# Performance work log

Hardware: AMD Instinct MI355X
Metric: run time of the kernel (lower is better)

The kernel has to match this reference:

```python
import jax, jax.numpy as jnp
import numpy as np

C = 256

def conv1x1(x, w, b):
    # pointwise Conv3d(kernel=1): out-channel d from in-channel c
    return jnp.einsum('blhwc,dc->blhwd', x, w) + b

def setup_inputs() -> dict:
    key = jax.random.key(0)
    ks = jax.random.split(key, 20)
    inp = {
        'x': jax.random.normal(ks[0], (2, 8, 64, 64, C + 3), jnp.float32),
        'mask': jnp.ones((2, 8, 64, 64), dtype=bool),
        'spatial_correction_matrix': jax.random.normal(ks[1], (2, 8, 4, 4), jnp.float32),
    }
    scale = 1.0 / np.sqrt(C)
    names = ['sq', 'sk', 'sv', 'tq', 'tk', 'tv']
    for i, n in enumerate(names):
        inp[n + '_w'] = jax.random.normal(ks[2 + 2 * i], (C, C), jnp.float32) * scale
        inp[n + '_b'] = jax.random.normal(ks[3 + 2 * i], (C,), jnp.float32) * 0.01
    inp['s_gamma'] = jax.random.normal(ks[14], (1,), jnp.float32) * 0.1
    inp['t_gamma'] = jax.random.normal(ks[15], (1,), jnp.float32) * 0.1
    return inp

def reference(x, mask, spatial_correction_matrix,
              sq_w, sq_b, sk_w, sk_b, sv_w, sv_b, s_gamma,
              tq_w, tq_b, tk_w, tk_b, tv_w, tv_b, t_gamma):
    x_s = x[..., :-3]                      # (B,L,H,W,C)
    B, L, H, W, Ch = x_s.shape
    prev = x_s                             # last_time == None -> last_time = x.detach()
    HW = H * W

    # ---- SpatialAttention: channel-attention (CxC) per (B,L) slice ----
    q = jnp.transpose(conv1x1(x_s, sq_w, sq_b), (0, 1, 4, 2, 3)).reshape(B * L, Ch, HW)
    k = jnp.transpose(conv1x1(x_s, sk_w, sk_b), (0, 1, 4, 2, 3)).reshape(B * L, Ch, HW)
    attn = jax.nn.softmax(jnp.einsum('bcs,bds->bcd', q, k), axis=-1)   # (BL,C,C)
    v = jnp.transpose(conv1x1(x_s, sv_w, sv_b), (0, 1, 4, 2, 3)).reshape(B * L, Ch, HW)
    out = jnp.einsum('bds,bcd->bsc', v, attn).reshape(B, L, H, W, Ch)
    x1 = s_gamma * out + x_s

    # ---- TemporalAttention: query from x1, key/value from prev ----
    q2 = jnp.transpose(conv1x1(x1, tq_w, tq_b), (0, 1, 4, 2, 3)).reshape(B * L, Ch, HW)
    # key: permute(0,2,1,4,3) swaps H/W before flatten (faithful to source)
    k2 = jnp.transpose(conv1x1(prev, tk_w, tk_b), (0, 1, 4, 3, 2)).reshape(B * L, Ch, HW)
    attn2 = jax.nn.softmax(jnp.einsum('bcs,bds->bcd', q2, k2), axis=-1)
    # value: reshape of (B,C,L,H,W)-contiguous tensor into (B*L,C,HW) scrambles C/L (faithful)
    v2 = jnp.transpose(conv1x1(prev, tv_w, tv_b), (0, 4, 1, 2, 3)).reshape(B * L, Ch, HW)
    out2 = jnp.einsum('bds,bcd->bsc', v2, attn2).reshape(B, L, H, W, Ch)
    x2 = t_gamma * out2 + x1
    return x2
```

## Files before the change

kernel.cpp:

```cpp
#include <hip/hip_runtime.h>
#include <stdint.h>


#define S4 4096
#define CH 256

typedef __attribute__((ext_vector_type(8))) short bf16x8;
typedef __attribute__((ext_vector_type(4))) float f32x4;

static __device__ __forceinline__ float bf2f(unsigned short u){
  union { unsigned int i; float f; } v; v.i = ((unsigned int)u) << 16; return v.f;
}
static __device__ __forceinline__ unsigned short f2bf(float f){
  union { float f; unsigned int i; } v; v.f = f;
  unsigned int x = v.i;
  x += 0x7fffu + ((x >> 16) & 1u);
  return (unsigned short)(x >> 16);
}
static __device__ __forceinline__ void gload16(const void* g, void* l){
  __builtin_amdgcn_global_load_lds((const __attribute__((address_space(1))) void*)g,
                                   (__attribute__((address_space(3))) void*)l, 16, 0, 0);
}


// ... 25 lines not shown

__global__ void k_wprep(const float* __restrict__ w0, const float* __restrict__ w1,
                        const float* __restrict__ w2, const float* __restrict__ w3,
                        const float* __restrict__ w4, const float* __restrict__ w5,
                        unsigned short* __restrict__ whi, unsigned short* __restrict__ wlo,
                        unsigned short* __restrict__ wvthi, unsigned short* __restrict__ wvtlo){
  int i = blockIdx.x*256 + threadIdx.x;
  int mat = i >> 16; int off = i & 65535;
  if (mat < 6){
    const float* src = mat==0?w0:mat==1?w1:mat==2?w2:mat==3?w3:mat==4?w4:w5;
    float v = src[off];
    unsigned short h = f2bf(v);
    whi[i] = h;
    wlo[i] = f2bf(v - bf2f(h));
  } else {
    int e = off >> 8, d = off & 255;
    float v = w2[d*256 + e];
    unsigned short h = f2bf(v);
    wvthi[off] = h;
    wvtlo[off] = f2bf(v - bf2f(h));
  }
}

__global__ void k_gcomb(const float* __restrict__ Gp,
                        unsigned short* __restrict__ ghi, unsigned short* __restrict__ glo){
  int bl = blockIdx.y;
  int idx = blockIdx.x*256 + threadIdx.x;
  float s = 0.f;
  #pragma unroll
  for (int p = 0; p < 8; ++p) s += Gp[(long)(bl*8 + p)*65536 + idx];
  unsigned short h = f2bf(s);
  ghi[(long)bl*65536 + idx] = h;
  glo[(long)bl*65536 + idx] = f2bf(s - bf2f(h));
}


template<bool BSWAP>
__global__ __launch_bounds__(256) void k_gram(
  const unsigned short* __restrict__ Xhi, const unsigned short* __restrict__ Xlo,
  float* __restrict__ Gp)
{
  __shared__ char lds[65536];
  char* ldsAh = lds;
  char* ldsAl = lds + 16384;
  char* ldsBh = lds + 32768;
  char* ldsBl = lds + 49152;
// ... 97 lines not shown
      }
    }
    __syncthreads();
    #pragma unroll
    for (int g2 = 0; g2 < 2; ++g2){
      int t2 = g2*256 + tid;
      int rr = t2 >> 4;
      int co = (t2 & 15) * 8;
      int mg = m0 + chv*32 + rr;
      int ng = n0 + co;
      long oidx = (long)zz*65536 + (long)mg*256 + ng;
      float4 o0, o1;
      o0.x = ldsF[rr*136+co+0]; o0.y = ldsF[rr*136+co+1];
      o0.z = ldsF[rr*136+co+2]; o0.w = ldsF[rr*136+co+3];
      o1.x = ldsF[rr*136+co+4]; o1.y = ldsF[rr*136+co+5];
      o1.z = ldsF[rr*136+co+6]; o1.w = ldsF[rr*136+co+7];
      *(float4*)(Gp + oidx)     = o0;
      *(float4*)(Gp + oidx + 4) = o1;
    }
  }
}


__device__ __forceinline__ void mega_tile(
  char* lds, int tid,
  const unsigned short* __restrict__ Ah, const unsigned short* __restrict__ Al,
  const unsigned short* __restrict__ Bh, const unsigned short* __restrict__ Bl,
  f32x4 acc[4][4])
{
  char* ldsAh = lds;
  char* ldsAl = lds + 32768;
  char* ldsBh = lds + 65536;
  char* ldsBl = lds + 81920;
  const int l = tid & 63, wid = tid >> 6;
  const int g = wid >> 2, w2 = wid & 3;
  const int wm = w2 >> 1, wn = w2 & 1;
  const int lm = l & 15, lk = l >> 4;
  const int fm = g*128 + wm*64, fn = wn*64;

  for (int kt = 0; kt < 4; ++kt){
    const int kq = kt << 6;
    #pragma unroll
    for (int it = 0; it < 4; ++it){
      int idx = it*512 + tid;
      int r = idx >> 3;
      int kb = ((idx & 7) << 4) ^ ((r & 7) << 4);
      long ga = (long)r*256 + kq + (kb >> 1);
      gload16(Ah + ga, ldsAh + idx*16);
      gload16(Al + ga, ldsAl + idx*16);
    }
    #pragma unroll
    for (int it = 0; it < 2; ++it){
      int idx = it*512 + tid;
      int r = idx >> 3;
      int kb = ((idx & 7) << 4) ^ ((r & 7) << 4);
      long gb = (long)r*256 + kq + (kb >> 1);
      gload16(Bh + gb, ldsBh + idx*16);
      gload16(Bl + gb, ldsBl + idx*16);
    }
    __syncthreads();
    #pragma unroll
    for (int kk = 0; kk < 2; ++kk){
      bf16x8 ah[4], al_[4];
      #pragma unroll
      for (int i=0;i<4;++i){
        int r = fm + i*16 + lm;
        int kb = ((kk<<6) + (lk<<4)) ^ ((r & 7) << 4);
        ah[i]  = *(const bf16x8*)(ldsAh + r*128 + kb);
        al_[i] = *(const bf16x8*)(ldsAl + r*128 + kb);
      }
      #pragma unroll
      for (int j=0;j<4;++j){
        int r = fn + j*16 + lm;
        int kb = ((kk<<6) + (lk<<4)) ^ ((r & 7) << 4);
        bf16x8 bh  = *(const bf16x8*)(ldsBh + r*128 + kb);
        bf16x8 bl8 = *(const bf16x8*)(ldsBl + r*128 + kb);
        #pragma unroll
        for (int i=0;i<4;++i){
          acc[i][j] = __builtin_amdgcn_mfma_f32_16x16x32_bf16(ah[i], bh, acc[i][j], 0, 0, 0);
          acc[i][j] = __builtin_amdgcn_mfma_f32_16x16x32_bf16(ah[i], bl8, acc[i][j], 0, 0, 0);
          acc[i][j] = __builtin_amdgcn_mfma_f32_16x16x32_bf16(al_[i], bh, acc[i][j], 0, 0, 0);
        }
      }
    }
    __syncthreads();
  }
}

template<int MODE>
__device__ __forceinline__ void mega_epi(
  char* lds, int tid, f32x4 acc[4][4], int bl, int n0, float gs,
  const float* ra1, const float* rb1, const float* ra2, const float* rb2,
  const float* pu, float* ph1,
  unsigned short* __restrict__ Oh, unsigned short* __restrict__ Ol,
  float* __restrict__ O32)
{
  const int l = tid & 63, wid = tid >> 6;
  const int g = wid >> 2, w2 = wid & 3;
  const int wm = w2 >> 1, wn = w2 & 1;
  const int lm = l & 15, lk = l >> 4;
  const int fnl = wn*64;
  float* ldsF = (float*)(lds + g*17408);
  const int tid2 = tid & 255;
  const int gr = tid >> 8;

  #pragma unroll
  for (int chv = 0; chv < 4; ++chv){
    __syncthreads();
    if (wm == (chv >> 1)){
      #pragma unroll
      for (int i2=0;i2<2;++i2){
        int i = (chv & 1)*2 + i2;
        #pragma unroll
        for (int j=0;j<4;++j){
          int n = fnl + j*16 + lm;
          int m2 = i2*16 + lk*4;
          #pragma unroll
          for (int r2=0;r2<4;++r2) ldsF[(m2+r2)*136 + n] = acc[i][j][r2];
        }
      }
    }
    __syncthreads();
    float* ldsFr = (float*)(lds + gr*17408);
    #pragma unroll
    for (int g2 = 0; g2 < 2; ++g2){
      int t2 = g2*256 + tid2;
      int rr = t2 >> 4;
      int co = (t2 & 15) * 8;
      float v[8];
      #pragma unroll
      for (int e=0;e<8;++e) v[e] = ldsFr[rr*136 + co + e];
      int mg = gr*128 + chv*32 + rr;
      int ng = n0 + co;
      long oidx = (long)bl*65536 + (long)mg*256 + ng;
      if (MODE == 1){
        float a1v = ra1[mg], a2v = ra2[mg];
        #pragma unroll
        for (int e=0;e<8;++e) v[e] += a1v*rb1[ng+e] + a2v*rb2[ng+e];
        float4 o0, o1;
        o0.x=v[0]; o0.y=v[1]; o0.z=v[2]; o0.w=v[3];
        o1.x=v[4]; o1.y=v[5]; o1.z=v[6]; o1.w=v[7];
        *(float4*)(O32 + oidx)     = o0;
        *(float4*)(O32 + oidx + 4) = o1;
      } else {
        if (MODE == 2){
          float hs = 0.f;
          #pragma unroll
          for (int e=0;e<8;++e){
            float w = ((mg == ng + e) ? 1.f : 0.f) + gs*v[e];
            hs += w * pu[ng+e];
            v[e] = w;
          }
          atomicAdd(&ph1[mg], hs);
        }
        if (MODE == 3){
          float a1v = ra1[mg];
          #pragma unroll
          for (int e=0;e<8;++e) v[e] += a1v * rb1[ng+e];
        }
        union { int4 vv; unsigned short u[8]; } hh, ll;
        #pragma unroll
        for (int e=0;e<8;++e) hh.u[e] = f2bf(v[e]);
        *(int4*)(Oh + oidx) = hh.vv;
        #pragma unroll
        for (int e=0;e<8;++e) ll.u[e] = f2bf(v[e] - bf2f(hh.u[e]));
        *(int4*)(Ol + oidx) = ll.vv;
      }
    }
  }
  __threadfence();
  __syncthreads();
}

template<int SMODE>
__device__ __forceinline__ void mega_softmax(
  int bl, int tid, const float* __restrict__ logits, float tg,
  const float* psvb, float* pc1,
  unsigned short* __restrict__ Oh, unsigned short* __restrict__ Ol)
{
  const int l = tid & 63, wid = tid >> 6;
  const long base = (long)bl*65536;
  for (int rr = 0; rr < 32; rr += 2){
    int c0 = wid*32 + rr;
    const float* p0 = logits + base + (long)c0*256 + l*4;
    float4 va = *(const float4*)p0;
    float4 vb = *(const float4*)(p0 + 256);
    float ma = fmaxf(fmaxf(va.x,va.y), fmaxf(va.z,va.w));
    float mb = fmaxf(fmaxf(vb.x,vb.y), fmaxf(vb.z,vb.w));
    #pragma unroll
    for (int off=32; off; off>>=1){
      ma = fmaxf(ma, __shfl_xor(ma, off, 64));
      mb = fmaxf(mb, __shfl_xor(mb, off, 64));
    }
    float ea0=__expf(va.x-ma), ea1=__expf(va.y-ma), ea2=__expf(va.z-ma), ea3=__expf(va.w-ma);
    float eb0=__expf(vb.x-mb), eb1=__expf(vb.y-mb), eb2=__expf(vb.z-mb), eb3=__expf(vb.w-mb);
    float sa = ea0+ea1+ea2+ea3, sb = eb0+eb1+eb2+eb3;
    float da = 0.f, db = 0.f;
    if (SMODE == 0){
      float4 bv = *(const float4*)(psvb + l*4);
      da = ea0*bv.x + ea1*bv.y + ea2*bv.z + ea3*bv.w;
      db = eb0*bv.x + eb1*bv.y + eb2*bv.z + eb3*bv.w;
    }
    #pragma unroll
    for (int off=32; off; off>>=1){
      sa += __shfl_xor(sa, off, 64);
      sb += __shfl_xor(sb, off, 64);
      if (SMODE == 0){ da += __shfl_xor(da, off, 64); db += __shfl_xor(db, off, 64); }
    }
    float ia = 1.f/sa, ib = 1.f/sb;
    if (SMODE == 1){ ia *= tg; ib *= tg; }
    float pa0=ea0*ia, pa1=ea1*ia, pa2=ea2*ia, pa3=ea3*ia;
    float pb0=eb0*ib, pb1v=eb1*ib, pb2=eb2*ib, pb3=eb3*ib;
    ushort4 h0, h1v;
    h0.x=f2bf(pa0); h0.y=f2bf(pa1); h0.z=f2bf(pa2); h0.w=f2bf(pa3);
    h1v.x=f2bf(pb0); h1v.y=f2bf(pb1v); h1v.z=f2bf(pb2); h1v.w=f2bf(pb3);
    *(ushort4*)(Oh + base + (long)c0*256 + l*4)     = h0;
    *(ushort4*)(Oh + base + (long)(c0+1)*256 + l*4) = h1v;
    if (SMODE == 0){
      ushort4 l0, l1v;
      l0.x=f2bf(pa0-bf2f(h0.x)); l0.y=f2bf(pa1-bf2f(h0.y));
      l0.z=f2bf(pa2-bf2f(h0.z)); l0.w=f2bf(pa3-bf2f(h0.w));
      l1v.x=f2bf(pb0-bf2f(h1v.x)); l1v.y=f2bf(pb1v-bf2f(h1v.y));
      l1v.z=f2bf(pb2-bf2f(h1v.z)); l1v.w=f2bf(pb3-bf2f(h1v.w));
      *(ushort4*)(Ol + base + (long)c0*256 + l*4)     = l0;
      *(ushort4*)(Ol + base + (long)(c0+1)*256 + l*4) = l1v;
      if (l == 0){ pc1[c0] = da*ia; pc1[c0+1] = db*ib; }
    }
  }
}

__global__ __launch_bounds__(512) void k_mega(
  const unsigned short* __restrict__ Whi, const unsigned short* __restrict__ Wlo,
  const unsigned short* __restrict__ WvThi, const unsigned short* __restrict__ WvTlo,
  const unsigned short* __restrict__ G1hi, const unsigned short* __restrict__ G1lo,
  const unsigned short* __restrict__ GShi, const unsigned short* __restrict__ GSlo,
  const float* __restrict__ sq_w, const float* __restrict__ sk_w,
  const float* __restrict__ tk_w, const float* __restrict__ tq_w,
  const float* __restrict__ sq_b, const float* __restrict__ sk_b,
  const float* __restrict__ sv_b, const float* __restrict__ tq_b,
  const float* __restrict__ tk_b,
  const float* __restrict__ s_gp, const float* __restrict__ t_gp,
  const float* __restrict__ u,
  unsigned short* __restrict__ Pth, unsigned short* __restrict__ Ptl,
  float* __restrict__ logits,
  unsigned short* __restrict__ a1h, unsigned short* __restrict__ a1l,
  unsigned short* __restrict__ W1h, unsigned short* __restrict__ W1l,
  unsigned short* __restrict__ G2h, unsigned short* __restrict__ G2l,
  unsigned short* __restrict__ a2g,
  float* __restrict__ b1eff_g)
{
  __shared__ char lds[111616];
  float* P = (float*)(lds + 98304);
  float* pu    = P;
  float* psqb  = P + 256;
  float* pskb  = P + 512;
  float* psvb  = P + 768;
  float* ptqb  = P + 1024;
  float* ptkb  = P + 1280;
  float* pwqu  = P + 1536;
  float* pwku  = P + 1792;
  float* pwtku = P + 2048;
  float* pwtqh = P + 2304;
  float* pc1   = P + 2560;
  float* ph1   = P + 2816;
  float* pb1   = P + 3072;

  const int tid = threadIdx.x;
  const int bl = blockIdx.x;
  const float gs = s_gp[0], tg = t_gp[0];
  const long gb = (long)bl*65536;

  if (tid < 256){
    pu[tid]   = u[bl*256 + tid];
    psqb[tid] = sq_b[tid];
    pskb[tid] = sk_b[tid];
    psvb[tid] = sv_b[tid];
    ptqb[tid] = tq_b[tid];
    ptkb[tid] = tk_b[tid];
    ph1[tid]  = 0.f;
  }
  __syncthreads();

  {
    int c = tid & 255, hh = tid >> 8;
    if (hh == 0){
      float s1 = 0.f, s2 = 0.f;
      #pragma unroll 4
      for (int e = 0; e < 256; e += 4){
        float4 w1_ = *(const float4*)(sq_w + c*256 + e);
        float4 w2_ = *(const float4*)(tk_w + c*256 + e);
        float u0=pu[e], u1=pu[e+1], u2=pu[e+2], u3=pu[e+3];
        s1 += w1_.x*u0 + w1_.y*u1 + w1_.z*u2 + w1_.w*u3;
        s2 += w2_.x*u0 + w2_.y*u1 + w2_.z*u2 + w2_.w*u3;
      }
      pwqu[c]  = s1 + 4096.f*psqb[c];
      pwtku[c] = s2;
    } else {
      float s = 0.f;
      #pragma unroll 4
      for (int e = 0; e < 256; e += 4){
        float4 w1_ = *(const float4*)(sk_w + c*256 + e);
        s += w1_.x*pu[e] + w1_.y*pu[e+1] + w1_.z*pu[e+2] + w1_.w*pu[e+3];
      }
      pwku[c] = s;
    }
    __syncthreads();
  }

  f32x4 acc[4][4];
  #define ZACC { for (int i_=0;i_<4;++i_) for (int j_=0;j_<4;++j_) acc[i_][j_]=(f32x4){0.f,0.f,0.f,0.f}; }

  for (int n0 = 0; n0 < 256; n0 += 128){
    ZACC;
    mega_tile(lds, tid, Whi + 65536, Wlo + 65536, G1hi + gb + n0*256, G1lo + gb + n0*256, acc);
    mega_epi<0>(lds, tid, acc, bl, n0, 0.f, nullptr,nullptr,nullptr,nullptr, pu, ph1, Pth, Ptl, nullptr);
  }
  for (int n0 = 0; n0 < 256; n0 += 128){
    ZACC;
    mega_tile(lds, tid, Whi, Wlo, Pth + gb + n0*256, Ptl + gb + n0*256, acc);
    mega_epi<1>(lds, tid, acc, bl, n0, 0.f, pwqu, pskb, psqb, pwku, pu, ph1, nullptr, nullptr, logits);
  }
  mega_softmax<0>(bl, tid, logits, 1.f, psvb, pc1, a1h, a1l);
  __threadfence();
  __syncthreads();
  for (int n0 = 0; n0 < 256; n0 += 128){
    ZACC;
    mega_tile(lds, tid, a1h + gb, a1l + gb, WvThi + n0*256, WvTlo + n0*256, acc);
    mega_epi<2>(lds, tid, acc, bl, n0, gs, nullptr,nullptr,nullptr,nullptr, pu, ph1, W1h, W1l, nullptr);
  }
  if (tid < 256){
    float b1 = gs * pc1[tid];
    pb1[tid] = b1;
    b1eff_g[bl*256 + tid] = b1;
    ph1[tid] = ph1[tid] + 4096.f*b1;
  }
  __syncthreads();
  if (tid < 256){
    int c = tid;
    float s = 0.f;
    #pragma unroll 4
    for (int e = 0; e < 256; e += 4){
      float4 w = *(const float4*)(tq_w + c*256 + e);
      s += w.x*ph1[e] + w.y*ph1[e+1] + w.z*ph1[e+2] + w.w*ph1[e+3];
    }
    pwtqh[c] = s + 4096.f*ptqb[c];
  }
  __syncthreads();
  for (int n0 = 0; n0 < 256; n0 += 128){
    ZACC;
    mega_tile(lds, tid, W1h + gb, W1l + gb, GShi + gb + n0*256, GSlo + gb + n0*256, acc);
    mega_epi<3>(lds, tid, acc, bl, n0, 0.f, pb1, pu, nullptr, nullptr, pu, ph1, G2h, G2l, nullptr);
  }
  for (int n0 = 0; n0 < 256; n0 += 128){
    ZACC;
    mega_tile(lds, tid, Whi + 4*65536, Wlo + 4*65536, G2h + gb + n0*256, G2l + gb + n0*256, acc);
    mega_epi<0>(lds, tid, acc, bl, n0, 0.f, nullptr,nullptr,nullptr,nullptr, pu, ph1, Pth, Ptl, nullptr);
  }
  for (int n0 = 0; n0 < 256; n0 += 128){
    ZACC;
    mega_tile(lds, tid, Whi + 3*65536, Wlo + 3*65536, Pth + gb + n0*256, Ptl + gb + n0*256, acc);
    mega_epi<1>(lds, tid, acc, bl, n0, 0.f, pwtqh, ptkb, ptqb, pwtku, pu, ph1, nullptr, nullptr, logits);
  }
  mega_softmax<1>(bl, tid, logits, tg, psvb, pc1, a2g, nullptr);
  #undef ZACC
}


template<bool SPLIT,int OUT_MODE>
__global__ __launch_bounds__(256) void k_gemm(
  const unsigned short* __restrict__ Ahi, const unsigned short* __restrict__ Alo,
  long Abl, int Ars,
  const unsigned short* __restrict__ Bhi, const unsigned short* __restrict__ Blo,
  long Bbl, int Brs,
  const float* __restrict__ bias,
  unsigned short* __restrict__ O16a,
  long Obl, int Ors)
{
  constexpr int LDSZ = 32768;
  __shared__ char lds[LDSZ];
  char* ldsAh = lds;
  char* ldsBh = lds + 16384;

  const int tid = threadIdx.x;
  const int l   = tid & 63;
  const int wid = tid >> 6;
  const int wm  = wid >> 1, wn = wid & 1;
  const int lm  = l & 15, lk = l >> 4;
  const int fm  = wm*64, fn = wn*64;
  const int bl  = blockIdx.z;
  const int m0  = blockIdx.x * 128;
  const int n0  = blockIdx.y * 128;

  f32x4 acc[4][4];
  #pragma unroll
  for (int i=0;i<4;++i)
    #pragma unroll
    for (int j=0;j<4;++j) acc[i][j] = (f32x4){0.f,0.f,0.f,0.f};

  for (int kt = 0; kt < 4; ++kt){
    const int kq = kt << 6;
    #pragma unroll
    for (int it=0; it<4; ++it){
      int idx = it*256 + tid;
      int r = idx >> 3;
      int kb = ((idx & 7) << 4) ^ ((r & 7) << 4);
      long ga = (long)bl*Abl + (long)(m0 + r)*Ars + kq + (kb >> 1);
      gload16(Ahi + ga, ldsAh + idx*16);
      long gbb = (long)bl*Bbl + (long)(n0 + r)*Brs + kq + (kb >> 1);
      gload16(Bhi + gbb, ldsBh + idx*16);
    }
    __syncthreads();
    #pragma unroll
    for (int kk=0; kk<2; ++kk){
      bf16x8 ah[4];
      #pragma unroll
      for (int i=0;i<4;++i){
        int r = fm + i*16 + lm;
        int kb = ((kk<<6) + (lk<<4)) ^ ((r & 7) << 4);
        ah[i] = *(const bf16x8*)(ldsAh + r*128 + kb);
      }
      #pragma unroll
      for (int j=0;j<4;++j){
        int r = fn + j*16 + lm;
        int kb = ((kk<<6) + (lk<<4)) ^ ((r & 7) << 4);
        bf16x8 bh = *(const bf16x8*)(ldsBh + r*128 + kb);
        #pragma unroll
        for (int i=0;i<4;++i)
          acc[i][j] = __builtin_amdgcn_mfma_f32_16x16x32_bf16(ah[i], bh, acc[i][j], 0, 0, 0);
      }
    }
    __syncthreads();
  }

  float* ldsF = (float*)lds;
  #pragma unroll
  for (int chv=0; chv<4; ++chv){
    __syncthreads();
    if (wm == (chv >> 1)){
      #pragma unroll
      for (int i2=0;i2<2;++i2){
        int i = (chv & 1)*2 + i2;
        #pragma unroll
        for (int j=0;j<4;++j){
          int n = fn + j*16 + lm;
          int m2 = i2*16 + lk*4;
          #pragma unroll
          for (int r2=0;r2<4;++r2) ldsF[(m2+r2)*136 + n] = acc[i][j][r2];
        }
      }
    }
    __syncthreads();
    #pragma unroll
    for (int g2=0; g2<2; ++g2){
      int t2 = g2*256 + tid;
      int rr = t2 >> 4;
      int co = (t2 & 15) * 8;
      float v[8];
      #pragma unroll
      for (int e=0;e<8;++e) v[e] = ldsF[rr*136 + co + e];
      int mg = m0 + chv*32 + rr;
      int ng = n0 + co;
      long oidx = (long)bl*Obl + (long)mg*Ors + ng;
      float b = bias ? bias[mg] : 0.f;
      union { int4 vv; unsigned short u[8]; } hh;
      #pragma unroll
      for (int e=0;e<8;++e) hh.u[e] = f2bf(v[e] + b);
      *(int4*)(O16a + oidx) = hh.vv;
    }
  }
}


__global__ __launch_bounds__(256,2) void k_final(
  const unsigned short* __restrict__ v2T,
  const unsigned short* __restrict__ attn2g,
  const unsigned short* __restrict__ Xhi, const unsigned short* __restrict__ Xlo,
  const unsigned short* __restrict__ W1hi, const unsigned short* __restrict__ W1lo,
  const float* __restrict__ b1eff,
  float* __restrict__ out)
{
  __shared__ char lds[32768];
  char* ldsA = lds; char* ldsB = lds + 16384;
  const int tid = threadIdx.x;
  const int l = tid & 63, wid = tid >> 6;
  const int wm = wid >> 1, wn = wid & 1;
  const int lm = l & 15, lk = l >> 4;
  const int fm = wm*64, fn = wn*64;
  const int bl = blockIdx.z;
  const int m0 = blockIdx.x*128;
// ... 136 lines not shown
  auto take = [&](size_t n){ char* r = p + off; off = (off + n + 255) & ~(size_t)255; return r; };

  unsigned short* Whi    = (unsigned short*)take((size_t)6*65536*2);
  unsigned short* Wlo    = (unsigned short*)take((size_t)6*65536*2);
  unsigned short* WvThi  = (unsigned short*)take((size_t)65536*2);
  unsigned short* WvTlo  = (unsigned short*)take((size_t)65536*2);
  unsigned short* Xhi    = (unsigned short*)take((size_t)16*S4*CH*2);
  unsigned short* Xlo    = (unsigned short*)take((size_t)16*S4*CH*2);
  unsigned short* v2T    = (unsigned short*)take((size_t)16*S4*CH*2);
  float*          Gp     = (float*)take((size_t)128*65536*4);
  unsigned short* G1hi   = (unsigned short*)take((size_t)16*65536*2);
  unsigned short* G1lo   = (unsigned short*)take((size_t)16*65536*2);
  unsigned short* GShi   = (unsigned short*)take((size_t)16*65536*2);
  unsigned short* GSlo   = (unsigned short*)take((size_t)16*65536*2);
  unsigned short* Pthi   = (unsigned short*)take((size_t)16*65536*2);
  unsigned short* Ptlo   = (unsigned short*)take((size_t)16*65536*2);
  unsigned short* G2hi   = (unsigned short*)take((size_t)16*65536*2);
  unsigned short* G2lo   = (unsigned short*)take((size_t)16*65536*2);
  unsigned short* W1hi   = (unsigned short*)take((size_t)16*65536*2);
  unsigned short* W1lo   = (unsigned short*)take((size_t)16*65536*2);
  unsigned short* a1hi   = (unsigned short*)take((size_t)16*65536*2);
  unsigned short* a1lo   = (unsigned short*)take((size_t)16*65536*2);
  unsigned short* a2g    = (unsigned short*)take((size_t)16*65536*2);
  float*          logits = (float*)take((size_t)16*65536*4);
  float*          ups    = (float*)take((size_t)1024*256*4);
  float*          u      = (float*)take((size_t)16*256*4);
  float*          b1eff  = (float*)take((size_t)16*256*4);

  const long XBL = (long)S4*CH;

  k_wprep<<<dim3(1792), 256, 0, stream>>>(sq_w, sk_w, sv_w, tq_w, tk_w, tv_w,
                                          Whi, Wlo, WvThi, WvTlo);
  k_xprep2<<<dim3(1024), 256, 0, stream>>>(x, Xhi, Xlo, ups);
  k_vecfin<<<dim3(16), 256, 0, stream>>>(ups, u);

  k_gram<false><<<dim3(2,2,128), 256, 0, stream>>>(Xhi, Xlo, Gp);
  k_gcomb<<<dim3(256,16), 256, 0, stream>>>(Gp, G1hi, G1lo);
  k_gram<true><<<dim3(2,2,128), 256, 0, stream>>>(Xhi, Xlo, Gp);
  k_gcomb<<<dim3(256,16), 256, 0, stream>>>(Gp, GShi, GSlo);

  k_mega<<<dim3(16), 512, 0, stream>>>(
     Whi, Wlo, WvThi, WvTlo, G1hi, G1lo, GShi, GSlo,
     sq_w, sk_w, tk_w, tq_w, sq_b, sk_b, sv_b, tq_b, tk_b,
     s_g, t_g, u,
     Pthi, Ptlo, logits, a1hi, a1lo, W1hi, W1lo, G2hi, G2lo, a2g, b1eff);

  k_gemm<false,1><<<dim3(2,32,16), 256, 0, stream>>>(
     Whi+5*65536, nullptr, 0, 256,  Xhi, nullptr, XBL, 256,
     tv_b, v2T, XBL, S4);

  k_final<<<dim3(32,2,16), 256, 0, stream>>>(v2T, a2g, Xhi, Xlo, W1hi, W1lo, b1eff, (float*)d_out);
}
```

Before: 607.9 us.

## Split 16-block mega kernel into multi-block channel GEMM and fused logit-softmax kernels

Replaces the monolithic k_mega, which ran one 512-thread block per (B,L) slice, with a chain of separate kernels: vector precompute kernels, a 64-block split-bf16 channel GEMM (k_cgemm), and a k_logit kernel that fuses the logit GEMM epilogue with the row softmax, so the fp32 logits buffer is no longer written and re-read. The aim is to occupy far more compute units than 16 blocks could on a large GPU. The cost is extra kernel launches and intermediate results round-tripping through global memory between stages, plus a global atomic accumulation for ph1 that now needs a memset beforehand.

```diff
diff --git a/kernel.cpp b/kernel.cpp
--- a/kernel.cpp
+++ b/kernel.cpp
@@ -71,6 +71,49 @@
   }
 }
 
+__global__ void k_vec1(const float* __restrict__ sq_w, const float* __restrict__ sq_b,
+                       const float* __restrict__ sk_w, const float* __restrict__ tk_w,
+                       const float* __restrict__ u,
+                       float* __restrict__ wqu, float* __restrict__ wku, float* __restrict__ wtku){
+  int bl = blockIdx.x, mat = blockIdx.y;
+  const float* W = mat==0? sq_w : mat==1? sk_w : tk_w;
+  int l = threadIdx.x & 63, w = threadIdx.x >> 6;
+  const float* ub = u + bl*256;
+  for (int i=0;i<64;++i){
+    int c = w*64 + i;
+    float s = 0.f;
+    #pragma unroll
+    for (int j=0;j<4;++j) s += W[c*256 + l + 64*j] * ub[l + 64*j];
+    #pragma unroll
+    for (int off=32; off; off>>=1) s += __shfl_xor(s, off, 64);
+    if (l==0){
+      if (mat==0) wqu [bl*256+c] = s + 4096.f*sq_b[c];
+      else if (mat==1) wku [bl*256+c] = s;
+      else wtku[bl*256+c] = s;
+    }
+  }
+}
+
+__global__ void k_vec2(const float* __restrict__ ph1_g, const float* __restrict__ c1_g,
+                       const float* __restrict__ s_gp,
+                       const float* __restrict__ tq_w, const float* __restrict__ tq_b,
+                       float* __restrict__ b1eff_g, float* __restrict__ wtqh){
+  __shared__ float h1[256];
+  int bl = blockIdx.x, tid = threadIdx.x;
+  float gs = s_gp[0];
+  float b1 = gs * c1_g[bl*256 + tid];
+  b1eff_g[bl*256 + tid] = b1;
+  h1[tid] = ph1_g[bl*256 + tid] + 4096.f*b1;
+  __syncthreads();
+  float s = 0.f;
+  #pragma unroll 4
+  for (int e = 0; e < 256; e += 4){
+    float4 w = *(const float4*)(tq_w + tid*256 + e);
+    s += w.x*h1[e] + w.y*h1[e+1] + w.z*h1[e+2] + w.w*h1[e+3];
+  }
+  wtqh[bl*256 + tid] = s + 4096.f*tq_b[tid];
+}
+
 __global__ void k_gcomb(const float* __restrict__ Gp,
                         unsigned short* __restrict__ ghi, unsigned short* __restrict__ glo){
   int bl = blockIdx.y;
@@ -214,364 +257,19 @@
 }
 
 
-__device__ __forceinline__ void mega_tile(
-  char* lds, int tid,
-  const unsigned short* __restrict__ Ah, const unsigned short* __restrict__ Al,
-  const unsigned short* __restrict__ Bh, const unsigned short* __restrict__ Bl,
-  f32x4 acc[4][4])
-{
-  char* ldsAh = lds;
-  char* ldsAl = lds + 32768;
-  char* ldsBh = lds + 65536;
-  char* ldsBl = lds + 81920;
-  const int l = tid & 63, wid = tid >> 6;
-  const int g = wid >> 2, w2 = wid & 3;
-  const int wm = w2 >> 1, wn = w2 & 1;
-  const int lm = l & 15, lk = l >> 4;
-  const int fm = g*128 + wm*64, fn = wn*64;
-
-  for (int kt = 0; kt < 4; ++kt){
-    const int kq = kt << 6;
-    #pragma unroll
-    for (int it = 0; it < 4; ++it){
-      int idx = it*512 + tid;
-      int r = idx >> 3;
-      int kb = ((idx & 7) << 4) ^ ((r & 7) << 4);
-      long ga = (long)r*256 + kq + (kb >> 1);
-      gload16(Ah + ga, ldsAh + idx*16);
-      gload16(Al + ga, ldsAl + idx*16);
-    }
-    #pragma unroll
-    for (int it = 0; it < 2; ++it){
-      int idx = it*512 + tid;
-      int r = idx >> 3;
-      int kb = ((idx & 7) << 4) ^ ((r & 7) << 4);
-      long gb = (long)r*256 + kq + (kb >> 1);
-      gload16(Bh + gb, ldsBh + idx*16);
-      gload16(Bl + gb, ldsBl + idx*16);
-    }
-    __syncthreads();
-    #pragma unroll
-    for (int kk = 0; kk < 2; ++kk){
-      bf16x8 ah[4], al_[4];
-      #pragma unroll
-      for (int i=0;i<4;++i){
-        int r = fm + i*16 + lm;
-        int kb = ((kk<<6) + (lk<<4)) ^ ((r & 7) << 4);
-        ah[i]  = *(const bf16x8*)(ldsAh + r*128 + kb);
-        al_[i] = *(const bf16x8*)(ldsAl + r*128 + kb);
-      }
-      #pragma unroll
-      for (int j=0;j<4;++j){
-        int r = fn + j*16 + lm;
-        int kb = ((kk<<6) + (lk<<4)) ^ ((r & 7) << 4);
-        bf16x8 bh  = *(const bf16x8*)(ldsBh + r*128 + kb);
-        bf16x8 bl8 = *(const bf16x8*)(ldsBl + r*128 + kb);
-        #pragma unroll
-        for (int i=0;i<4;++i){
-          acc[i][j] = __builtin_amdgcn_mfma_f32_16x16x32_bf16(ah[i], bh, acc[i][j], 0, 0, 0);
-          acc[i][j] = __builtin_amdgcn_mfma_f32_16x16x32_bf16(ah[i], bl8, acc[i][j], 0, 0, 0);
-          acc[i][j] = __builtin_amdgcn_mfma_f32_16x16x32_bf16(al_[i], bh, acc[i][j], 0, 0, 0);
-        }
-      }
-    }
-    __syncthreads();
-  }
-}
-
-template<int MODE>
-__device__ __forceinline__ void mega_epi(
-  char* lds, int tid, f32x4 acc[4][4], int bl, int n0, float gs,
-  const float* ra1, const float* rb1, const float* ra2, const float* rb2,
-  const float* pu, float* ph1,
-  unsigned short* __restrict__ Oh, unsigned short* __restrict__ Ol,
-  float* __restrict__ O32)
-{
-  const int l = tid & 63, wid = tid >> 6;
-  const int g = wid >> 2, w2 = wid & 3;
-  const int wm = w2 >> 1, wn = w2 & 1;
-  const int lm = l & 15, lk = l >> 4;
-  const int fnl = wn*64;
-  float* ldsF = (float*)(lds + g*17408);
-  const int tid2 = tid & 255;
-  const int gr = tid >> 8;
-
-  #pragma unroll
-  for (int chv = 0; chv < 4; ++chv){
-    __syncthreads();
-    if (wm == (chv >> 1)){
-      #pragma unroll
-      for (int i2=0;i2<2;++i2){
-        int i = (chv & 1)*2 + i2;
-        #pragma unroll
-        for (int j=0;j<4;++j){
-          int n = fnl + j*16 + lm;
-          int m2 = i2*16 + lk*4;
-          #pragma unroll
-          for (int r2=0;r2<4;++r2) ldsF[(m2+r2)*136 + n] = acc[i][j][r2];
-        }
-      }
-    }
-    __syncthreads();
-    float* ldsFr = (float*)(lds + gr*17408);
-    #pragma unroll
-    for (int g2 = 0; g2 < 2; ++g2){
-      int t2 = g2*256 + tid2;
-      int rr = t2 >> 4;
-      int co = (t2 & 15) * 8;
-      float v[8];
-      #pragma unroll
-      for (int e=0;e<8;++e) v[e] = ldsFr[rr*136 + co + e];
-      int mg = gr*128 + chv*32 + rr;
-      int ng = n0 + co;
-      long oidx = (long)bl*65536 + (long)mg*256 + ng;
-      if (MODE == 1){
-        float a1v = ra1[mg], a2v = ra2[mg];
-        #pragma unroll
-        for (int e=0;e<8;++e) v[e] += a1v*rb1[ng+e] + a2v*rb2[ng+e];
-        float4 o0, o1;
-        o0.x=v[0]; o0.y=v[1]; o0.z=v[2]; o0.w=v[3];
-        o1.x=v[4]; o1.y=v[5]; o1.z=v[6]; o1.w=v[7];
-        *(float4*)(O32 + oidx)     = o0;
-        *(float4*)(O32 + oidx + 4) = o1;
-      } else {
-        if (MODE == 2){
-          float hs = 0.f;
-          #pragma unroll
-          for (int e=0;e<8;++e){
-            float w = ((mg == ng + e) ? 1.f : 0.f) + gs*v[e];
-            hs += w * pu[ng+e];
-            v[e] = w;
-          }
-          atomicAdd(&ph1[mg], hs);
-        }
-        if (MODE == 3){
-          float a1v = ra1[mg];
-          #pragma unroll
-          for (int e=0;e<8;++e) v[e] += a1v * rb1[ng+e];
-        }
-        union { int4 vv; unsigned short u[8]; } hh, ll;
-        #pragma unroll
-        for (int e=0;e<8;++e) hh.u[e] = f2bf(v[e]);
-        *(int4*)(Oh + oidx) = hh.vv;
-        #pragma unroll
-        for (int e=0;e<8;++e) ll.u[e] = f2bf(v[e] - bf2f(hh.u[e]));
-        *(int4*)(Ol + oidx) = ll.vv;
-      }
-    }
-  }
-  __threadfence();
-  __syncthreads();
-}
-
-template<int SMODE>
-__device__ __forceinline__ void mega_softmax(
-  int bl, int tid, const float* __restrict__ logits, float tg,
-  const float* psvb, float* pc1,
+template<int OUT_MODE>
+__global__ __launch_bounds__(256) void k_cgemm(
+  const unsigned short* __restrict__ Ah, const unsigned short* __restrict__ Al, long Abl,
+  const unsigned short* __restrict__ Bh, const unsigned short* __restrict__ Bl, long Bbl,
+  const float* __restrict__ ra1, int ra1st, const float* __restrict__ rb1, int rb1st,
+  const float* __restrict__ gsp, const float* __restrict__ u_g, float* __restrict__ ph1_g,
   unsigned short* __restrict__ Oh, unsigned short* __restrict__ Ol)
 {
-  const int l = tid & 63, wid = tid >> 6;
-  const long base = (long)bl*65536;
-  for (int rr = 0; rr < 32; rr += 2){
-    int c0 = wid*32 + rr;
-    const float* p0 = logits + base + (long)c0*256 + l*4;
-    float4 va = *(const float4*)p0;
-    float4 vb = *(const float4*)(p0 + 256);
-    float ma = fmaxf(fmaxf(va.x,va.y), fmaxf(va.z,va.w));
-    float mb = fmaxf(fmaxf(vb.x,vb.y), fmaxf(vb.z,vb.w));
-    #pragma unroll
-    for (int off=32; off; off>>=1){
-      ma = fmaxf(ma, __shfl_xor(ma, off, 64));
-      mb = fmaxf(mb, __shfl_xor(mb, off, 64));
-    }
-    float ea0=__expf(va.x-ma), ea1=__expf(va.y-ma), ea2=__expf(va.z-ma), ea3=__expf(va.w-ma);
-    float eb0=__expf(vb.x-mb), eb1=__expf(vb.y-mb), eb2=__expf(vb.z-mb), eb3=__expf(vb.w-mb);
-    float sa = ea0+ea1+ea2+ea3, sb = eb0+eb1+eb2+eb3;
-    float da = 0.f, db = 0.f;
-    if (SMODE == 0){
-      float4 bv = *(const float4*)(psvb + l*4);
-      da = ea0*bv.x + ea1*bv.y + ea2*bv.z + ea3*bv.w;
-      db = eb0*bv.x + eb1*bv.y + eb2*bv.z + eb3*bv.w;
-    }
-    #pragma unroll
-    for (int off=32; off; off>>=1){
-      sa += __shfl_xor(sa, off, 64);
-      sb += __shfl_xor(sb, off, 64);
-      if (SMODE == 0){ da += __shfl_xor(da, off, 64); db += __shfl_xor(db, off, 64); }
-    }
-    float ia = 1.f/sa, ib = 1.f/sb;
-    if (SMODE == 1){ ia *= tg; ib *= tg; }
-    float pa0=ea0*ia, pa1=ea1*ia, pa2=ea2*ia, pa3=ea3*ia;
-    float pb0=eb0*ib, pb1v=eb1*ib, pb2=eb2*ib, pb3=eb3*ib;
-    ushort4 h0, h1v;
-    h0.x=f2bf(pa0); h0.y=f2bf(pa1); h0.z=f2bf(pa2); h0.w=f2bf(pa3);
-    h1v.x=f2bf(pb0); h1v.y=f2bf(pb1v); h1v.z=f2bf(pb2); h1v.w=f2bf(pb3);
-    *(ushort4*)(Oh + base + (long)c0*256 + l*4)     = h0;
-    *(ushort4*)(Oh + base + (long)(c0+1)*256 + l*4) = h1v;
-    if (SMODE == 0){
-      ushort4 l0, l1v;
-      l0.x=f2bf(pa0-bf2f(h0.x)); l0.y=f2bf(pa1-bf2f(h0.y));
-      l0.z=f2bf(pa2-bf2f(h0.z)); l0.w=f2bf(pa3-bf2f(h0.w));
-      l1v.x=f2bf(pb0-bf2f(h1v.x)); l1v.y=f2bf(pb1v-bf2f(h1v.y));
-      l1v.z=f2bf(pb2-bf2f(h1v.z)); l1v.w=f2bf(pb3-bf2f(h1v.w));
-      *(ushort4*)(Ol + base + (long)c0*256 + l*4)     = l0;
-      *(ushort4*)(Ol + base + (long)(c0+1)*256 + l*4) = l1v;
-      if (l == 0){ pc1[c0] = da*ia; pc1[c0+1] = db*ib; }
-    }
-  }
-}
-
-__global__ __launch_bounds__(512) void k_mega(
-  const unsigned short* __restrict__ Whi, const unsigned short* __restrict__ Wlo,
-  const unsigned short* __restrict__ WvThi, const unsigned short* __restrict__ WvTlo,
-  const unsigned short* __restrict__ G1hi, const unsigned short* __restrict__ G1lo,
-  const unsigned short* __restrict__ GShi, const unsigned short* __restrict__ GSlo,
-  const float* __restrict__ sq_w, const float* __restrict__ sk_w,
-  const float* __restrict__ tk_w, const float* __restrict__ tq_w,
-  const float* __restrict__ sq_b, const float* __restrict__ sk_b,
-  const float* __restrict__ sv_b, const float* __restrict__ tq_b,
-  const float* __restrict__ tk_b,
-  const float* __restrict__ s_gp, const float* __restrict__ t_gp,
-  const float* __restrict__ u,
-  unsigned short* __restrict__ Pth, unsigned short* __restrict__ Ptl,
-  float* __restrict__ logits,
-  unsigned short* __restrict__ a1h, unsigned short* __restrict__ a1l,
-  unsigned short* __restrict__ W1h, unsigned short* __restrict__ W1l,
-  unsigned short* __restrict__ G2h, unsigned short* __restrict__ G2l,
-  unsigned short* __restrict__ a2g,
-  float* __restrict__ b1eff_g)
-{
-  __shared__ char lds[111616];
-  float* P = (float*)(lds + 98304);
-  float* pu    = P;
-  float* psqb  = P + 256;
-  float* pskb  = P + 512;
-  float* psvb  = P + 768;
-  float* ptqb  = P + 1024;
-  float* ptkb  = P + 1280;
-  float* pwqu  = P + 1536;
-  float* pwku  = P + 1792;
-  float* pwtku = P + 2048;
-  float* pwtqh = P + 2304;
-  float* pc1   = P + 2560;
-  float* ph1   = P + 2816;
-  float* pb1   = P + 3072;
-
-  const int tid = threadIdx.x;
-  const int bl = blockIdx.x;
-  const float gs = s_gp[0], tg = t_gp[0];
-  const long gb = (long)bl*65536;
-
-  if (tid < 256){
-    pu[tid]   = u[bl*256 + tid];
-    psqb[tid] = sq_b[tid];
-    pskb[tid] = sk_b[tid];
-    psvb[tid] = sv_b[tid];
-    ptqb[tid] = tq_b[tid];
-    ptkb[tid] = tk_b[tid];
-    ph1[tid]  = 0.f;
-  }
-  __syncthreads();
-
-  {
-    int c = tid & 255, hh = tid >> 8;
-    if (hh == 0){
-      float s1 = 0.f, s2 = 0.f;
-      #pragma unroll 4
-      for (int e = 0; e < 256; e += 4){
-        float4 w1_ = *(const float4*)(sq_w + c*256 + e);
-        float4 w2_ = *(const float4*)(tk_w + c*256 + e);
-        float u0=pu[e], u1=pu[e+1], u2=pu[e+2], u3=pu[e+3];
-        s1 += w1_.x*u0 + w1_.y*u1 + w1_.z*u2 + w1_.w*u3;
-        s2 += w2_.x*u0 + w2_.y*u1 + w2_.z*u2 + w2_.w*u3;
-      }
-      pwqu[c]  = s1 + 4096.f*psqb[c];
-      pwtku[c] = s2;
-    } else {
-      float s = 0.f;
-      #pragma unroll 4
-      for (int e = 0; e < 256; e += 4){
-        float4 w1_ = *(const float4*)(sk_w + c*256 + e);
-        s += w1_.x*pu[e] + w1_.y*pu[e+1] + w1_.z*pu[e+2] + w1_.w*pu[e+3];
-      }
-      pwku[c] = s;
-    }
-    __syncthreads();
-  }
-
-  f32x4 acc[4][4];
-  #define ZACC { for (int i_=0;i_<4;++i_) for (int j_=0;j_<4;++j_) acc[i_][j_]=(f32x4){0.f,0.f,0.f,0.f}; }
-
-  for (int n0 = 0; n0 < 256; n0 += 128){
-    ZACC;
-    mega_tile(lds, tid, Whi + 65536, Wlo + 65536, G1hi + gb + n0*256, G1lo + gb + n0*256, acc);
-    mega_epi<0>(lds, tid, acc, bl, n0, 0.f, nullptr,nullptr,nullptr,nullptr, pu, ph1, Pth, Ptl, nullptr);
-  }
-  for (int n0 = 0; n0 < 256; n0 += 128){
-    ZACC;
-    mega_tile(lds, tid, Whi, Wlo, Pth + gb + n0*256, Ptl + gb + n0*256, acc);
-    mega_epi<1>(lds, tid, acc, bl, n0, 0.f, pwqu, pskb, psqb, pwku, pu, ph1, nullptr, nullptr, logits);
-  }
-  mega_softmax<0>(bl, tid, logits, 1.f, psvb, pc1, a1h, a1l);
-  __threadfence();
-  __syncthreads();
-  for (int n0 = 0; n0 < 256; n0 += 128){
-    ZACC;
-    mega_tile(lds, tid, a1h + gb, a1l + gb, WvThi + n0*256, WvTlo + n0*256, acc);
-    mega_epi<2>(lds, tid, acc, bl, n0, gs, nullptr,nullptr,nullptr,nullptr, pu, ph1, W1h, W1l, nullptr);
-  }
-  if (tid < 256){
-    float b1 = gs * pc1[tid];
-    pb1[tid] = b1;
-    b1eff_g[bl*256 + tid] = b1;
-    ph1[tid] = ph1[tid] + 4096.f*b1;
-  }
-  __syncthreads();
-  if (tid < 256){
-    int c = tid;
-    float s = 0.f;
-    #pragma unroll 4
-    for (int e = 0; e < 256; e += 4){
-      float4 w = *(const float4*)(tq_w + c*256 + e);
-      s += w.x*ph1[e] + w.y*ph1[e+1] + w.z*ph1[e+2] + w.w*ph1[e+3];
-    }
-    pwtqh[c] = s + 4096.f*ptqb[c];
-  }
-  __syncthreads();
-  for (int n0 = 0; n0 < 256; n0 += 128){
-    ZACC;
-    mega_tile(lds, tid, W1h + gb, W1l + gb, GShi + gb + n0*256, GSlo + gb + n0*256, acc);
-    mega_epi<3>(lds, tid, acc, bl, n0, 0.f, pb1, pu, nullptr, nullptr, pu, ph1, G2h, G2l, nullptr);
-  }
-  for (int n0 = 0; n0 < 256; n0 += 128){
-    ZACC;
-    mega_tile(lds, tid, Whi + 4*65536, Wlo + 4*65536, G2h + gb + n0*256, G2l + gb + n0*256, acc);
-    mega_epi<0>(lds, tid, acc, bl, n0, 0.f, nullptr,nullptr,nullptr,nullptr, pu, ph1, Pth, Ptl, nullptr);
-  }
-  for (int n0 = 0; n0 < 256; n0 += 128){
-    ZACC;
-    mega_tile(lds, tid, Whi + 3*65536, Wlo + 3*65536, Pth + gb + n0*256, Ptl + gb + n0*256, acc);
-    mega_epi<1>(lds, tid, acc, bl, n0, 0.f, pwtqh, ptkb, ptqb, pwtku, pu, ph1, nullptr, nullptr, logits);
-  }
-  mega_softmax<1>(bl, tid, logits, tg, psvb, pc1, a2g, nullptr);
-  #undef ZACC
-}
-
-
-template<bool SPLIT,int OUT_MODE>
-__global__ __launch_bounds__(256) void k_gemm(
-  const unsigned short* __restrict__ Ahi, const unsigned short* __restrict__ Alo,
-  long Abl, int Ars,
-  const unsigned short* __restrict__ Bhi, const unsigned short* __restrict__ Blo,
-  long Bbl, int Brs,
-  const float* __restrict__ bias,
-  unsigned short* __restrict__ O16a,
-  long Obl, int Ors)
-{
-  constexpr int LDSZ = 32768;
-  __shared__ char lds[LDSZ];
+  __shared__ char lds[65536];
   char* ldsAh = lds;
-  char* ldsBh = lds + 16384;
+  char* ldsAl = lds + 16384;
+  char* ldsBh = lds + 32768;
+  char* ldsBl = lds + 49152;
 
   const int tid = threadIdx.x;
   const int l   = tid & 63;
@@ -596,34 +294,42 @@
       int idx = it*256 + tid;
       int r = idx >> 3;
       int kb = ((idx & 7) << 4) ^ ((r & 7) << 4);
-      long ga = (long)bl*Abl + (long)(m0 + r)*Ars + kq + (kb >> 1);
-      gload16(Ahi + ga, ldsAh + idx*16);
-      long gbb = (long)bl*Bbl + (long)(n0 + r)*Brs + kq + (kb >> 1);
-      gload16(Bhi + gbb, ldsBh + idx*16);
+      long ga = (long)bl*Abl + (long)(m0 + r)*256 + kq + (kb >> 1);
+      gload16(Ah + ga, ldsAh + idx*16);
+      gload16(Al + ga, ldsAl + idx*16);
+      long gbb = (long)bl*Bbl + (long)(n0 + r)*256 + kq + (kb >> 1);
+      gload16(Bh + gbb, ldsBh + idx*16);
+      gload16(Bl + gbb, ldsBl + idx*16);
     }
     __syncthreads();
     #pragma unroll
     for (int kk=0; kk<2; ++kk){
-      bf16x8 ah[4];
+      bf16x8 ah[4], al_[4];
       #pragma unroll
       for (int i=0;i<4;++i){
         int r = fm + i*16 + lm;
         int kb = ((kk<<6) + (lk<<4)) ^ ((r & 7) << 4);
-        ah[i] = *(const bf16x8*)(ldsAh + r*128 + kb);
+        ah[i]  = *(const bf16x8*)(ldsAh + r*128 + kb);
+        al_[i] = *(const bf16x8*)(ldsAl + r*128 + kb);
       }
       #pragma unroll
       for (int j=0;j<4;++j){
         int r = fn + j*16 + lm;
         int kb = ((kk<<6) + (lk<<4)) ^ ((r & 7) << 4);
-        bf16x8 bh = *(const bf16x8*)(ldsBh + r*128 + kb);
-        #pragma unroll
-        for (int i=0;i<4;++i)
+        bf16x8 bh  = *(const bf16x8*)(ldsBh + r*128 + kb);
+        bf16x8 bl8 = *(const bf16x8*)(ldsBl + r*128 + kb);
+        #pragma unroll
+        for (int i=0;i<4;++i){
           acc[i][j] = __builtin_amdgcn_mfma_f32_16x16x32_bf16(ah[i], bh, acc[i][j], 0, 0, 0);
-      }
-    }
-    __syncthreads();
-  }
-
+          acc[i][j] = __builtin_amdgcn_mfma_f32_16x16x32_bf16(ah[i], bl8, acc[i][j], 0, 0, 0);
+          acc[i][j] = __builtin_amdgcn_mfma_f32_16x16x32_bf16(al_[i], bh, acc[i][j], 0, 0, 0);
+        }
+      }
+    }
+    __syncthreads();
+  }
+
+  float gs = (OUT_MODE==2) ? gsp[0] : 0.f;
   float* ldsF = (float*)lds;
   #pragma unroll
   for (int chv=0; chv<4; ++chv){
@@ -652,11 +358,274 @@
       for (int e=0;e<8;++e) v[e] = ldsF[rr*136 + co + e];
       int mg = m0 + chv*32 + rr;
       int ng = n0 + co;
-      long oidx = (long)bl*Obl + (long)mg*Ors + ng;
-      float b = bias ? bias[mg] : 0.f;
-      union { int4 vv; unsigned short u[8]; } hh;
-      #pragma unroll
-      for (int e=0;e<8;++e) hh.u[e] = f2bf(v[e] + b);
+      long oidx = (long)bl*65536 + (long)mg*256 + ng;
+      if (OUT_MODE == 0){
+        if (ra1){
+          float a1v = ra1[bl*ra1st + mg];
+          #pragma unroll
+          for (int e=0;e<8;++e) v[e] += a1v * rb1[bl*rb1st + ng + e];
+        }
+      }
+      if (OUT_MODE == 2){
+        float hs = 0.f;
+        #pragma unroll
+        for (int e=0;e<8;++e){
+          float w = ((mg == ng + e) ? 1.f : 0.f) + gs*v[e];
+          hs += w * u_g[bl*256 + ng + e];
+          v[e] = w;
+        }
+        atomicAdd(ph1_g + bl*256 + mg, hs);
+      }
+      union { int4 vv; unsigned short us[8]; } hh, ll;
+      #pragma unroll
+      for (int e=0;e<8;++e) hh.us[e] = f2bf(v[e]);
+      *(int4*)(Oh + oidx) = hh.vv;
+      #pragma unroll
+      for (int e=0;e<8;++e) ll.us[e] = f2bf(v[e] - bf2f(hh.us[e]));
+      *(int4*)(Ol + oidx) = ll.vv;
+    }
+  }
+}
+
+
+template<int SMODE>
+__global__ __launch_bounds__(512) void k_logit(
+  const unsigned short* __restrict__ Ah, const unsigned short* __restrict__ Al,
+  const unsigned short* __restrict__ Bh, const unsigned short* __restrict__ Bl,
+  const float* __restrict__ ra1, int ra1st, const float* __restrict__ rb1, int rb1st,
+  const float* __restrict__ ra2, int ra2st, const float* __restrict__ rb2, int rb2st,
+  const float* __restrict__ bvp, const float* __restrict__ tgp,
+  float* __restrict__ c1_g,
+  unsigned short* __restrict__ Oh, unsigned short* __restrict__ Ol)
+{
+  __shared__ char lds[98304];
+  char* ldsAh = lds;
+  char* ldsAl = lds + 16384;
+  char* ldsBh = lds + 32768;
+  char* ldsBl = lds + 65536;
+
+  const int tid = threadIdx.x;
+  const int l   = tid & 63;
+  const int wid = tid >> 6;
+  const int wm  = wid >> 2, wn = wid & 3;
+  const int lm  = l & 15, lk = l >> 4;
+  const int fm  = wm*64, fn = wn*64;
+  const int bl  = blockIdx.z;
+  const int m0  = blockIdx.x * 128;
+
+  f32x4 acc[4][4];
+  #pragma unroll
+  for (int i=0;i<4;++i)
+    #pragma unroll
+    for (int j=0;j<4;++j) acc[i][j] = (f32x4){0.f,0.f,0.f,0.f};
+
+  for (int kt = 0; kt < 4; ++kt){
+    const int kq = kt << 6;
+    #pragma unroll
+    for (int it=0; it<2; ++it){
+      int idx = it*512 + tid;
+      int r = idx >> 3;
+      int kb = ((idx & 7) << 4) ^ ((r & 7) << 4);
+      long ga = (long)(m0 + r)*256 + kq + (kb >> 1);
+      gload16(Ah + ga, ldsAh + idx*16);
+      gload16(Al + ga, ldsAl + idx*16);
+    }
+    #pragma unroll
+    for (int it=0; it<4; ++it){
+      int idx = it*512 + tid;
+      int r = idx >> 3;
+      int kb = ((idx & 7) << 4) ^ ((r & 7) << 4);
+      long gbb = (long)bl*65536 + (long)r*256 + kq + (kb >> 1);
+      gload16(Bh + gbb, ldsBh + idx*16);
+      gload16(Bl + gbb, ldsBl + idx*16);
+    }
+    __syncthreads();
+    #pragma unroll
+    for (int kk=0; kk<2; ++kk){
+      bf16x8 ah[4], al_[4];
+      #pragma unroll
+      for (int i=0;i<4;++i){
+        int r = fm + i*16 + lm;
+        int kb = ((kk<<6) + (lk<<4)) ^ ((r & 7) << 4);
+        ah[i]  = *(const bf16x8*)(ldsAh + r*128 + kb);
+        al_[i] = *(const bf16x8*)(ldsAl + r*128 + kb);
+      }
+      #pragma unroll
+      for (int j=0;j<4;++j){
+        int r = fn + j*16 + lm;
+        int kb = ((kk<<6) + (lk<<4)) ^ ((r & 7) << 4);
+        bf16x8 bh  = *(const bf16x8*)(ldsBh + r*128 + kb);
+        bf16x8 bl8 = *(const bf16x8*)(ldsBl + r*128 + kb);
+        #pragma unroll
+        for (int i=0;i<4;++i){
+          acc[i][j] = __builtin_amdgcn_mfma_f32_16x16x32_bf16(ah[i], bh, acc[i][j], 0, 0, 0);
+          acc[i][j] = __builtin_amdgcn_mfma_f32_16x16x32_bf16(ah[i], bl8, acc[i][j], 0, 0, 0);
+          acc[i][j] = __builtin_amdgcn_mfma_f32_16x16x32_bf16(al_[i], bh, acc[i][j], 0, 0, 0);
+        }
+      }
+    }
+    __syncthreads();
+  }
+
+  const float tg = (SMODE==1) ? tgp[0] : 1.f;
+  float* ldsF = (float*)lds;
+  #pragma unroll
+  for (int chv=0; chv<4; ++chv){
+    __syncthreads();
+    if (wm == (chv >> 1)){
+      #pragma unroll
+      for (int i2=0;i2<2;++i2){
+        int i = (chv & 1)*2 + i2;
+        #pragma unroll
+        for (int j=0;j<4;++j){
+          int n = fn + j*16 + lm;
+          int m2 = i2*16 + lk*4;
+          #pragma unroll
+          for (int r2=0;r2<4;++r2) ldsF[(m2+r2)*264 + n] = acc[i][j][r2];
+        }
+      }
+    }
+    __syncthreads();
+    {
+      int rr  = tid >> 4;
+      int ng0 = (tid & 15) * 16;
+      int mg  = m0 + chv*32 + rr;
+      float v[16];
+      #pragma unroll
+      for (int e=0;e<16;++e) v[e] = ldsF[rr*264 + ng0 + e];
+      float a1v = ra1[bl*ra1st + mg];
+      float a2v = ra2[bl*ra2st + mg];
+      #pragma unroll
+      for (int e=0;e<16;++e)
+        v[e] += a1v*rb1[bl*rb1st + ng0 + e] + a2v*rb2[bl*rb2st + ng0 + e];
+      float mx = v[0];
+      #pragma unroll
+      for (int e=1;e<16;++e) mx = fmaxf(mx, v[e]);
+      #pragma unroll
+      for (int off=1; off<16; off<<=1) mx = fmaxf(mx, __shfl_xor(mx, off, 64));
+      float sum = 0.f, dot = 0.f;
+      #pragma unroll
+      for (int e=0;e<16;++e){
+        v[e] = __expf(v[e] - mx);
+        sum += v[e];
+        if (SMODE == 0) dot += v[e] * bvp[ng0 + e];
+      }
+      #pragma unroll
+      for (int off=1; off<16; off<<=1){
+        sum += __shfl_xor(sum, off, 64);
+        if (SMODE == 0) dot += __shfl_xor(dot, off, 64);
+      }
+      float inv = tg / sum;
+      long oidx = (long)bl*65536 + (long)mg*256 + ng0;
+      union { int4 vv; unsigned short us[8]; } hh, ll;
+      #pragma unroll
+      for (int half=0; half<2; ++half){
+        #pragma unroll
+        for (int e=0;e<8;++e) hh.us[e] = f2bf(v[half*8+e] * inv);
+        *(int4*)(Oh + oidx + half*8) = hh.vv;
+        if (SMODE == 0){
+          #pragma unroll
+          for (int e=0;e<8;++e) ll.us[e] = f2bf(v[half*8+e]*inv - bf2f(hh.us[e]));
+          *(int4*)(Ol + oidx + half*8) = ll.vv;
+        }
+      }
+      if (SMODE == 0 && (tid & 15) == 0) c1_g[bl*256 + mg] = dot / sum;
+    }
+  }
+}
+
+
+__global__ __launch_bounds__(256) void k_vconv(
+  const unsigned short* __restrict__ Ah,
+  const unsigned short* __restrict__ Bh,
+  const float* __restrict__ bias,
+  unsigned short* __restrict__ O16a)
+{
+  __shared__ char lds[32768];
+  char* ldsAh = lds;
+  char* ldsBh = lds + 16384;
+
+  const int tid = threadIdx.x;
+  const int l   = tid & 63;
+  const int wid = tid >> 6;
+  const int wm  = wid >> 1, wn = wid & 1;
+  const int lm  = l & 15, lk = l >> 4;
+  const int fm  = wm*64, fn = wn*64;
+  const int bl  = blockIdx.z;
+  const int m0  = blockIdx.x * 128;
+  const int n0  = blockIdx.y * 128;
+
+  f32x4 acc[4][4];
+  #pragma unroll
+  for (int i=0;i<4;++i)
+    #pragma unroll
+    for (int j=0;j<4;++j) acc[i][j] = (f32x4){0.f,0.f,0.f,0.f};
+
+  for (int kt = 0; kt < 4; ++kt){
+    const int kq = kt << 6;
+    #pragma unroll
+    for (int it=0; it<4; ++it){
+      int idx = it*256 + tid;
+      int r = idx >> 3;
+      int kb = ((idx & 7) << 4) ^ ((r & 7) << 4);
+      long ga = (long)(m0 + r)*256 + kq + (kb >> 1);
+      gload16(Ah + ga, ldsAh + idx*16);
+      long gbb = (long)bl*1048576 + (long)(n0 + r)*256 + kq + (kb >> 1);
+      gload16(Bh + gbb, ldsBh + idx*16);
+    }
+    __syncthreads();
+    #pragma unroll
+    for (int kk=0; kk<2; ++kk){
+      bf16x8 ah[4];
+      #pragma unroll
+      for (int i=0;i<4;++i){
+        int r = fm + i*16 + lm;
+        int kb = ((kk<<6) + (lk<<4)) ^ ((r & 7) << 4);
+        ah[i] = *(const bf16x8*)(ldsAh + r*128 + kb);
+      }
+      #pragma unroll
+      for (int j=0;j<4;++j){
+        int r = fn + j*16 + lm;
+        int kb = ((kk<<6) + (lk<<4)) ^ ((r & 7) << 4);
+        bf16x8 bh = *(const bf16x8*)(ldsBh + r*128 + kb);
+        #pragma unroll
+        for (int i=0;i<4;++i)
+          acc[i][j] = __builtin_amdgcn_mfma_f32_16x16x32_bf16(ah[i], bh, acc[i][j], 0, 0, 0);
+      }
+    }
+    __syncthreads();
+  }
+
+  float* ldsF = (float*)lds;
+  #pragma unroll
+  for (int chv=0; chv<4; ++chv){
+    __syncthreads();
+    if (wm == (chv >> 1)){
+      #pragma unroll
+      for (int i2=0;i2<2;++i2){
+        int i = (chv & 1)*2 + i2;
+        #pragma unroll
+        for (int j=0;j<4;++j){
+          int n = fn + j*16 + lm;
+          int m2 = i2*16 + lk*4;
+          #pragma unroll
+          for (int r2=0;r2<4;++r2) ldsF[(m2+r2)*136 + n] = acc[i][j][r2];
+        }
+      }
+    }
+    __syncthreads();
+    #pragma unroll
+    for (int g2=0; g2<2; ++g2){
+      int t2 = g2*256 + tid;
+      int rr = t2 >> 4;
+      int co = (t2 & 15) * 8;
+      int mg = m0 + chv*32 + rr;
+      int ng = n0 + co;
+      long oidx = (long)bl*1048576 + (long)mg*4096 + ng;
+      float b = bias[mg];
+      union { int4 vv; unsigned short us[8]; } hh;
+      #pragma unroll
+      for (int e=0;e<8;++e) hh.us[e] = f2bf(ldsF[rr*136 + co + e] + b);
       *(int4*)(O16a + oidx) = hh.vv;
     }
   }
@@ -839,32 +808,52 @@
   unsigned short* a1hi   = (unsigned short*)take((size_t)16*65536*2);
   unsigned short* a1lo   = (unsigned short*)take((size_t)16*65536*2);
   unsigned short* a2g    = (unsigned short*)take((size_t)16*65536*2);
-  float*          logits = (float*)take((size_t)16*65536*4);
   float*          ups    = (float*)take((size_t)1024*256*4);
   float*          u      = (float*)take((size_t)16*256*4);
+  float*          wqu    = (float*)take((size_t)16*256*4);
+  float*          wku    = (float*)take((size_t)16*256*4);
+  float*          wtku   = (float*)take((size_t)16*256*4);
+  float*          c1_g   = (float*)take((size_t)16*256*4);
+  float*          ph1_g  = (float*)take((size_t)16*256*4);
   float*          b1eff  = (float*)take((size_t)16*256*4);
-
-  const long XBL = (long)S4*CH;
+  float*          wtqh   = (float*)take((size_t)16*256*4);
+
+  hipMemsetAsync(ph1_g, 0, (size_t)16*256*4, stream);
 
   k_wprep<<<dim3(1792), 256, 0, stream>>>(sq_w, sk_w, sv_w, tq_w, tk_w, tv_w,
                                           Whi, Wlo, WvThi, WvTlo);
   k_xprep2<<<dim3(1024), 256, 0, stream>>>(x, Xhi, Xlo, ups);
   k_vecfin<<<dim3(16), 256, 0, stream>>>(ups, u);
+  k_vec1<<<dim3(16,3), 256, 0, stream>>>(sq_w, sq_b, sk_w, tk_w, u, wqu, wku, wtku);
 
   k_gram<false><<<dim3(2,2,128), 256, 0, stream>>>(Xhi, Xlo, Gp);
   k_gcomb<<<dim3(256,16), 256, 0, stream>>>(Gp, G1hi, G1lo);
   k_gram<true><<<dim3(2,2,128), 256, 0, stream>>>(Xhi, Xlo, Gp);
   k_gcomb<<<dim3(256,16), 256, 0, stream>>>(Gp, GShi, GSlo);
 
-  k_mega<<<dim3(16), 512, 0, stream>>>(
-     Whi, Wlo, WvThi, WvTlo, G1hi, G1lo, GShi, GSlo,
-     sq_w, sk_w, tk_w, tq_w, sq_b, sk_b, sv_b, tq_b, tk_b,
-     s_g, t_g, u,
-     Pthi, Ptlo, logits, a1hi, a1lo, W1hi, W1lo, G2hi, G2lo, a2g, b1eff);
-
-  k_gemm<false,1><<<dim3(2,32,16), 256, 0, stream>>>(
-     Whi+5*65536, nullptr, 0, 256,  Xhi, nullptr, XBL, 256,
-     tv_b, v2T, XBL, S4);
+  k_vconv<<<dim3(2,32,16), 256, 0, stream>>>(Whi+5*65536, Xhi, tv_b, v2T);
+
+  k_cgemm<0><<<dim3(2,2,16), 256, 0, stream>>>(
+     Whi+1*65536, Wlo+1*65536, 0,  G1hi, G1lo, 65536,
+     nullptr,0, nullptr,0, nullptr, nullptr, nullptr, Pthi, Ptlo);
+  k_logit<0><<<dim3(2,1,16), 512, 0, stream>>>(
+     Whi, Wlo, Pthi, Ptlo,
+     wqu,256, sk_b,0, sq_b,0, wku,256,
+     sv_b, nullptr, c1_g, a1hi, a1lo);
+  k_cgemm<2><<<dim3(2,2,16), 256, 0, stream>>>(
+     a1hi, a1lo, 65536,  WvThi, WvTlo, 0,
+     nullptr,0, nullptr,0, s_g, u, ph1_g, W1hi, W1lo);
+  k_vec2<<<dim3(16), 256, 0, stream>>>(ph1_g, c1_g, s_g, tq_w, tq_b, b1eff, wtqh);
+  k_cgemm<0><<<dim3(2,2,16), 256, 0, stream>>>(
+     W1hi, W1lo, 65536,  GShi, GSlo, 65536,
+     b1eff,256, u,256, nullptr, nullptr, nullptr, G2hi, G2lo);
+  k_cgemm<0><<<dim3(2,2,16), 256, 0, stream>>>(
+     Whi+4*65536, Wlo+4*65536, 0,  G2hi, G2lo, 65536,
+     nullptr,0, nullptr,0, nullptr, nullptr, nullptr, Pthi, Ptlo);
+  k_logit<1><<<dim3(2,1,16), 512, 0, stream>>>(
+     Whi+3*65536, Wlo+3*65536, Pthi, Ptlo,
+     wtqh,256, tk_b,0, tq_b,0, wtku,256,
+     sv_b, t_g, nullptr, a2g, a2g);
 
   k_final<<<dim3(32,2,16), 256, 0, stream>>>(v2T, a2g, Xhi, Xlo, W1hi, W1lo, b1eff, (float*)d_out);
 }
```

Measured after the change: 499.0 us. -17.9%, faster.
